# Optimization experiments

Hardware: AMD Instinct MI355X
Metric: run time of the kernel (lower is better)

Reference implementation:

```python
import jax, jax.numpy as jnp
import numpy as np

LN_EPS = 1e-5

def _ln(x, g):
    # LayerNorm with no bias, matching torch (population variance)
    m = x.mean(-1, keepdims=True)
    v = x.var(-1, keepdims=True)
    return (x - m) / jnp.sqrt(v + LN_EPS) * g


def setup_inputs() -> dict:
    key = jax.random.key(0)
    ks = jax.random.split(key, 10)
    B, S, D, L, V = 4, 4096, 256, 6, 32000
    std = 0.02  # nn.init.normal_(std=0.02)
    tokens = jax.random.randint(ks[0], (B, S), 0, V)
    wte = jax.random.normal(ks[1], (V, D), jnp.float32) * std
    wpe = jax.random.normal(ks[2], (S + 1, D), jnp.float32) * std  # context_size+1 table
    g_e = jnp.ones((D,), jnp.float32)
    g_p = jnp.ones((D,), jnp.float32)
    g_out = jnp.ones((D,), jnp.float32)
    ff_w1 = jax.random.normal(ks[3], (D, 4 * D), jnp.float32) * std
    ff_w2 = jax.random.normal(ks[4], (4 * D, D), jnp.float32) * std
    Wq = jax.random.normal(ks[5], (L, D, D), jnp.float32) * std
    Wk = jax.random.normal(ks[6], (L, D, D), jnp.float32) * std
    Wv = jax.random.normal(ks[7], (L, D, D), jnp.float32) * std
    return {"tokens": tokens, "wte": wte, "wpe": wpe, "g_e": g_e, "g_p": g_p,
            "g_out": g_out, "ff_w1": ff_w1, "ff_w2": ff_w2,
            "Wq": Wq, "Wk": Wk, "Wv": Wv}


def reference(tokens, wte, wpe, g_e, g_p, g_out, ff_w1, ff_w2, Wq, Wk, Wv):
    B, S = tokens.shape
    D = wte.shape[1]
    L = Wq.shape[0]
    # embeddings + pre-LN (dropout = identity at eval)
    e = _ln(wte[tokens], g_e)                 # [B,S,D] token stream
    p = _ln(wpe[:S], g_p)                     # [S,D]   positional stream (batch-invariant)
    x = e + p[None]                           # [B,S,D]
    # covariate FF on positional stream (use_ppe=True): p = p + W2 @ gelu(W1 @ p)
    p = p + jax.nn.gelu(p @ ff_w1, approximate=False) @ ff_w2
    causal = jnp.tril(jnp.ones((S, S), bool))
    inv_sqrt_d = D ** -0.5
    for l in range(L):
        # use_ppe: Q=K from positional stream (batch-invariant), V from token embeds
        q = p @ Wq[l]                          # [S,D]
        k = p @ Wk[l]                          # [S,D]
        v = jnp.einsum('bsd,de->bse', e, Wv[l])  # [B,S,D]
        s = (q @ k.T) * inv_sqrt_d             # [S,S], shared across batch
        s = jnp.where(causal, s, -jnp.inf)
        a = jax.nn.softmax(s, axis=-1)
        x = x + jnp.einsum('st,btd->bsd', a, v)
    # targets=None path: last position only
    x = x[:, -1:, :]                           # [B,1,D]
    x = _ln(x, g_out)                          # use_ln_out
    logits = x @ _ln(wte, g_e).T               # tied output head through ln_e
    return logits                              # [B,1,V]
```

## Files before the change

kernel.cpp:

```cpp
#include <hip/hip_runtime.h>
#include <hip/hip_bf16.h>

#define LN_EPS 1e-5f

typedef __attribute__((ext_vector_type(8))) short s8v;
typedef __attribute__((ext_vector_type(4))) float f32x4;

__device__ __forceinline__ float wred_sum(float v) {
#pragma unroll
  for (int o = 32; o > 0; o >>= 1) v += __shfl_xor(v, o, 64);
  return v;
}
__device__ __forceinline__ float wred_max(float v) {
#pragma unroll
  for (int o = 32; o > 0; o >>= 1) v = fmaxf(v, __shfl_xor(v, o, 64));
  return v;
}
__device__ __forceinline__ float bf2f(unsigned short u) {
  union { unsigned int i; float f; } c;
  c.i = ((unsigned int)u) << 16;
  return c.f;
}
__device__ __forceinline__ unsigned short f2bf(float f) {
  __hip_bfloat16 h = (__hip_bfloat16)f;
  return *(unsigned short*)&h;
}
__device__ __forceinline__ float4 bf4(ushort4 u) {
  return (float4){bf2f(u.x), bf2f(u.y), bf2f(u.z), bf2f(u.w)};
}
__device__ __forceinline__ void async_cp16(const __hip_bfloat16* g, __hip_bfloat16* l) {
  __builtin_amdgcn_global_load_lds(
      (const __attribute__((address_space(1))) unsigned int*)g,
      (__attribute__((address_space(3))) unsigned int*)l, 16, 0, 0);
}

__global__ void prep_k(const float* __restrict__ wpe, const float* __restrict__ wte,
                       const int* __restrict__ tokens,
                       const float* __restrict__ g_p, const float* __restrict__ g_e,
                       const float* __restrict__ ff_w1,
                       unsigned short* __restrict__ p0b, unsigned short* __restrict__ e,
                       unsigned short* __restrict__ w1T, float* __restrict__ zeros) {
  __shared__ float lds[64][65];
  int bx = blockIdx.x, t = threadIdx.x;
  int w = t >> 6, lane = t & 63;

  if (bx < 5120) {
    int row;
    const float* g;
    const float4* src;
    if (bx < 1024) {
      row = bx * 4 + w;
      src = (const float4*)(wpe + (size_t)row * 256);
      g = g_p;
    } else {
      row = (bx - 1024) * 4 + w;
      int tok = tokens[row];
      src = (const float4*)(wte + (size_t)tok * 256);
      g = g_e;
    }
    float4 v = src[lane];
    float mean = wred_sum(v.x + v.y + v.z + v.w) * (1.f / 256.f);
    float4 d = {v.x - mean, v.y - mean, v.z - mean, v.w - mean};
    float var = wred_sum(d.x * d.x + d.y * d.y + d.z * d.z + d.w * d.w) * (1.f / 256.f);
    float r = rsqrtf(var + LN_EPS);
    float4 gv = ((const float4*)g)[lane];
    ushort4 ob = {f2bf(d.x * r * gv.x), f2bf(d.y * r * gv.y),
                  f2bf(d.z * r * gv.z), f2bf(d.w * r * gv.w)};
    if (bx < 1024) ((ushort4*)(p0b + (size_t)row * 256))[lane] = ob;
    else           ((ushort4*)(e   + (size_t)row * 256))[lane] = ob;
    return;
  }
  if (bx < 5184) {
    int i = bx - 5120;
    int bxx = i & 3, byy = i >> 2;
    int x = t & 63, y4 = t >> 6;
    int r0 = bxx * 64, c0 = byy * 64;
#pragma unroll
    for (int k = 0; k < 16; ++k) {
      int r = y4 * 16 + k;
      lds[r][x] = ff_w1[(size_t)(r0 + r) * 1024 + c0 + x];
    }
    __syncthreads();
#pragma unroll
    for (int k = 0; k < 16; ++k) {
      int a = y4 * 16 + k;
      w1T[(size_t)(c0 + a) * 256 + r0 + x] = f2bf(lds[x][a]);
    }
    return;
  }
  for (int i = t; i < 8960; i += 256) zeros[i] = 0.f;
}

__global__ __launch_bounds__(256, 4) void mfma_gemm_mlp(
    const __hip_bfloat16* __restrict__ A, const __hip_bfloat16* __restrict__ BT,
    __hip_bfloat16* __restrict__ Cout,
    const float* __restrict__ W2, const unsigned short* __restrict__ p0b,
    float* __restrict__ plast) {
  __shared__ __hip_bfloat16 As[64 * 64];
  __shared__ __hip_bfloat16 Bs[64 * 64];
  __shared__ float hl[64];
  const int t = threadIdx.x;
  const int lane = t & 63, wave = t >> 6;
  const int wr = wave >> 1, wc = wave & 1;
  const int fr = lane & 15, quad = lane >> 4;
  const int mtx = blockIdx.x, ntx = blockIdx.y;
  const int m0 = mtx * 64, n0 = ntx * 64;

  f32x4 acc[2][2];
#pragma unroll
  for (int i = 0; i < 2; ++i)
#pragma unroll
    for (int j = 0; j < 2; ++j) acc[i][j] = (f32x4){0.f, 0.f, 0.f, 0.f};

  for (int k0 = 0; k0 < 256; k0 += 64) {
    __syncthreads();
#pragma unroll
    for (int j = 0; j < 2; ++j) {
      int ld = wave * 2 + j;
      int slot = ld * 64 + lane;
      int m = slot >> 3, c = slot & 7;
      async_cp16(A + (size_t)(m0 + m) * 256 + k0 + ((c ^ (m & 7)) << 3), As + ld * 512);
    }
#pragma unroll
    for (int j = 0; j < 2; ++j) {
      int ld = wave * 2 + j;
      int slot = ld * 64 + lane;
      int n = slot >> 3, c = slot & 7;
      async_cp16(BT + (size_t)(n0 + n) * 256 + k0 + ((c ^ (n & 7)) << 3), Bs + ld * 512);
    }
    __syncthreads();
#pragma unroll
    for (int h = 0; h < 2; ++h) {
      s8v af[2], bfv[2];
#pragma unroll
      for (int i = 0; i < 2; ++i) {
        int m = wr * 32 + i * 16 + fr;
        int ch = (h * 4 + quad) ^ (m & 7);
        af[i] = *(const s8v*)(As + m * 64 + ch * 8);
      }
#pragma unroll
      for (int j = 0; j < 2; ++j) {
        int n = wc * 32 + j * 16 + fr;
        int ch = (h * 4 + quad) ^ (n & 7);
        bfv[j] = *(const s8v*)(Bs + n * 64 + ch * 8);
      }
#pragma unroll
      for (int i = 0; i < 2; ++i)
#pragma unroll
        for (int j = 0; j < 2; ++j)
          acc[i][j] = __builtin_amdgcn_mfma_f32_16x16x32_bf16(af[i], bfv[j], acc[i][j], 0, 0, 0);
    }
  }

#pragma unroll
  for (int i = 0; i < 2; ++i) {
#pragma unroll
    for (int j = 0; j < 2; ++j) {
#pragma unroll
      for (int r = 0; r < 4; ++r) {
        int row = m0 + wr * 32 + i * 16 + quad * 4 + r;
        int col = n0 + wc * 32 + j * 16 + fr;
        float v = acc[i][j][r];
        v = 0.5f * v * (1.f + erff(v * 0.70710678118654752f));
        Cout[(size_t)row * 1024 + col] = (__hip_bfloat16)v;
        if (mtx == 63 && row == 4095) hl[col - n0] = v;
      }
    }
  }
  if (mtx == 63) {
    __syncthreads();
    float pa = (ntx == 0) ? bf2f(p0b[(size_t)4095 * 256 + t]) : 0.f;
#pragma unroll
    for (int kk = 0; kk < 64; ++kk)
      pa += hl[kk] * W2[(size_t)(n0 + kk) * 256 + t];
    atomicAdd(&plast[t], pa);
  }
}

__global__ void q_k(const float* __restrict__ plast, const float* __restrict__ Wq,
                    float* __restrict__ qall) {
  int c = blockIdx.x, l = blockIdx.y, t = threadIdx.x;
  const float* W = Wq + (size_t)l * 65536;
  float pa = 0.f;
#pragma unroll
  for (int i = 0; i < 16; ++i) {
    int d = c * 16 + i;
    pa += plast[d] * W[d * 256 + t];
  }
  atomicAdd(&qall[l * 256 + t], pa);
}

__global__ void kv_k(const float* __restrict__ Wk, const float* __restrict__ qall,
                     float* __restrict__ kv) {
  int l = blockIdx.y;
  int w = threadIdx.x >> 6, lane = threadIdx.x & 63;
  int r = blockIdx.x * 4 + w;
  float4 wv = ((const float4*)(Wk + (size_t)l * 65536 + (size_t)r * 256))[lane];
  float4 qv = ((const float4*)(qall + l * 256))[lane];
  float dot = wred_sum(wv.x * qv.x + wv.y * qv.y + wv.z * qv.z + wv.w * qv.w);
  if (lane == 0) kv[l * 256 + r] = dot;
}

__global__ void w2kv_k(const float* __restrict__ W2, const float* __restrict__ kv,
                       float* __restrict__ w2kv) {
  int l = blockIdx.y;
  int w = threadIdx.x >> 6, lane = threadIdx.x & 63;
  int r = blockIdx.x * 4 + w;
  float4 wv = ((const float4*)(W2 + (size_t)r * 256))[lane];
  float4 qv = ((const float4*)(kv + l * 256))[lane];
  float dot = wred_sum(wv.x * qv.x + wv.y * qv.y + wv.z * qv.z + wv.w * qv.w);
  if (lane == 0) w2kv[l * 1024 + r] = dot;
}

__global__ __launch_bounds__(256) void sc_k(
    const unsigned short* __restrict__ p0b, const unsigned short* __restrict__ hB,
    const float* __restrict__ kv, const float* __restrict__ w2kv,
    float* __restrict__ sc) {
  __shared__ float skv[6 * 256];
  __shared__ float sw2[6 * 1024];
  int t = threadIdx.x;
  for (int i = t; i < 1536; i += 256) skv[i] = kv[i];
  for (int i = t; i < 6144; i += 256) sw2[i] = w2kv[i];
  __syncthreads();
  int wave = t >> 6, lane = t & 63;
#pragma unroll
  for (int rr = 0; rr < 2; ++rr) {
    int row = blockIdx.x * 8 + wave * 2 + rr;
    const ushort4* hrow = (const ushort4*)(hB + (size_t)row * 1024);
    float4 h0 = bf4(hrow[lane]);
    float4 h1 = bf4(hrow[64 + lane]);
    float4 h2 = bf4(hrow[128 + lane]);
    float4 h3 = bf4(hrow[192 + lane]);
    float4 p = bf4(((const ushort4*)(p0b + (size_t)row * 256))[lane]);
#pragma unroll
    for (int l = 0; l < 6; ++l) {
      float4 kf = ((const float4*)(skv + l * 256))[lane];
      float4 w0 = ((const float4*)(sw2 + l * 1024))[lane];
      float4 w1 = ((const float4*)(sw2 + l * 1024 + 256))[lane];
      float4 w2 = ((const float4*)(sw2 + l * 1024 + 512))[lane];
      float4 w3 = ((const float4*)(sw2 + l * 1024 + 768))[lane];
      float a = p.x * kf.x + p.y * kf.y + p.z * kf.z + p.w * kf.w;
      a += h0.x * w0.x + h0.y * w0.y + h0.z * w0.z + h0.w * w0.w;
      a += h1.x * w1.x + h1.y * w1.y + h1.z * w1.z + h1.w * w1.w;
      a += h2.x * w2.x + h2.y * w2.y + h2.z * w2.z + h2.w * w2.w;
      a += h3.x * w3.x + h3.y * w3.y + h3.z * w3.z + h3.w * w3.w;
      a = wred_sum(a);
      if (lane == 0) sc[(size_t)l * 4096 + row] = a * 0.0625f;
    }
  }
}

__global__ void softmax_k(const float* __restrict__ sc, float* __restrict__ w) {
  int l = blockIdx.x, t = threadIdx.x;
  float4 v = ((const float4*)(sc + (size_t)l * 4096))[t];
  float m = fmaxf(fmaxf(v.x, v.y), fmaxf(v.z, v.w));
  m = wred_max(m);
  __shared__ float red[16];
  __shared__ float red2[16];
  int lane = t & 63, wv = t >> 6;
  if (lane == 0) red[wv] = m;
  __syncthreads();
  float mm = red[0];
#pragma unroll
  for (int i = 1; i < 16; ++i) mm = fmaxf(mm, red[i]);
  float e0 = expf(v.x - mm), e1 = expf(v.y - mm), e2 = expf(v.z - mm), e3 = expf(v.w - mm);
  float s = wred_sum(e0 + e1 + e2 + e3);
  if (lane == 0) red2[wv] = s;
  __syncthreads();
  float tot = 0.f;
#pragma unroll
  for (int i = 0; i < 16; ++i) tot += red2[i];
  float inv = 1.f / tot;
  float4 o = {e0 * inv, e1 * inv, e2 * inv, e3 * inv};
  ((float4*)(w + (size_t)l * 4096))[t] = o;
}

__global__ void ctx_k(const unsigned short* __restrict__ e, const float* __restrict__ w,
                      float* __restrict__ ctx) {
  int c = blockIdx.x, b = blockIdx.y, t = threadIdx.x;
  const unsigned short* eb = e + ((size_t)b * 4096 + c * 32) * 256;
  const float* w0 = w + c * 32;
  float a[6] = {0.f, 0.f, 0.f, 0.f, 0.f, 0.f};
#pragma unroll 4
  for (int i = 0; i < 32; ++i) {
    float ev = bf2f(eb[(size_t)i * 256 + t]);
#pragma unroll
    for (int l = 0; l < 6; ++l) a[l] += w0[l * 4096 + i] * ev;
  }
#pragma unroll
  for (int l = 0; l < 6; ++l) atomicAdd(&ctx[(l * 4 + b) * 256 + t], a[l]);
}

__global__ void proj_k(const float* __restrict__ ctx, const float* __restrict__ Wv,
                       float* __restrict__ xacc) {
  int c = blockIdx.x, l = blockIdx.y, t = threadIdx.x;
  const float* W = Wv + (size_t)l * 65536;
  float pa[4] = {0.f, 0.f, 0.f, 0.f};
#pragma unroll
  for (int i = 0; i < 16; ++i) {
    int d = c * 16 + i;
    float wv = W[d * 256 + t];
#pragma unroll
    for (int b = 0; b < 4; ++b) pa[b] += ctx[(l * 4 + b) * 256 + d] * wv;
  }
#pragma unroll
  for (int b = 0; b < 4; ++b) atomicAdd(&xacc[b * 256 + t], pa[b]);
}

__global__ void logits_fin_k(const float* __restrict__ wte, const float* __restrict__ ge,
                             const float* __restrict__ gout,
                             const unsigned short* __restrict__ e,
                             const unsigned short* __restrict__ p0b,
                             const float* __restrict__ xacc,
                             float* __restrict__ out) {
  int wv = threadIdx.x >> 6, lane = threadIdx.x & 63;
  float4 go4 = ((const float4*)gout)[lane];
  float4 ge4 = ((const float4*)ge)[lane];
  float4 pl = bf4(((const ushort4*)(p0b + (size_t)4095 * 256))[lane]);
  float4 xb[4];
#pragma unroll
  for (int b = 0; b < 4; ++b) {
    float4 xa = ((const float4*)(xacc + b * 256))[lane];
    float4 ev = bf4(((const ushort4*)(e + ((size_t)(b * 4096 + 4095)) * 256))[lane]);
    float4 vv = {xa.x + ev.x + pl.x, xa.y + ev.y + pl.y,
                 xa.z + ev.z + pl.z, xa.w + ev.w + pl.w};
    float mean = wred_sum(vv.x + vv.y + vv.z + vv.w) * (1.f / 256.f);
    float4 d = {vv.x - mean, vv.y - mean, vv.z - mean, vv.w - mean};
    float var = wred_sum(d.x * d.x + d.y * d.y + d.z * d.z + d.w * d.w) * (1.f / 256.f);
    float r = rsqrtf(var + LN_EPS);
    xb[b] = (float4){d.x * r * go4.x, d.y * r * go4.y, d.z * r * go4.z, d.w * r * go4.w};
  }
  int v = blockIdx.x * 4 + wv;
  float4 x = ((const float4*)(wte + (size_t)v * 256))[lane];
  float mean = wred_sum(x.x + x.y + x.z + x.w) * (1.f / 256.f);
  float4 d = {x.x - mean, x.y - mean, x.z - mean, x.w - mean};
  float var = wred_sum(d.x * d.x + d.y * d.y + d.z * d.z + d.w * d.w) * (1.f / 256.f);
  float r = rsqrtf(var + LN_EPS);
  float4 ln = {d.x * r * ge4.x, d.y * r * ge4.y, d.z * r * ge4.z, d.w * r * ge4.w};
#pragma unroll
  for (int b = 0; b < 4; ++b) {
    float dot = wred_sum(ln.x * xb[b].x + ln.y * xb[b].y +
                         ln.z * xb[b].z + ln.w * xb[b].w);
    if (lane == 0) out[b * 32000 + v] = dot;
  }
}

#define O_E     ((size_t)0)
#define O_P0B   ((size_t)2097152)
#define O_W1T   ((size_t)2621440)
#define O_HB    ((size_t)2752512)
#define O_CTX   ((size_t)4849664)
#define O_QALL  ((size_t)4855808)
#define O_XACC  ((size_t)4857344)
#define O_PLAST ((size_t)4858368)
#define O_KV    ((size_t)4858624)
#define O_W2KV  ((size_t)4860160)
#define O_SC    ((size_t)4866304)
#define O_WSM   ((size_t)4890880)

extern "C" void kernel_launch(void* const* d_in, const int* in_sizes, int n_in,
                              void* d_out, int out_size, void* d_ws, size_t ws_size,
                              hipStream_t stream) {
  const int*   tokens = (const int*)d_in[0];
  const float* wte    = (const float*)d_in[1];
  const float* wpe    = (const float*)d_in[2];
  const float* g_e    = (const float*)d_in[3];
  const float* g_p    = (const float*)d_in[4];
  const float* g_out  = (const float*)d_in[5];
  const float* ff_w1  = (const float*)d_in[6];
  const float* ff_w2  = (const float*)d_in[7];
  const float* Wq     = (const float*)d_in[8];
  const float* Wk     = (const float*)d_in[9];
  const float* Wv     = (const float*)d_in[10];
  float* out = (float*)d_out;
  float* ws = (float*)d_ws;

  unsigned short* e   = (unsigned short*)(ws + O_E);
  unsigned short* p0b = (unsigned short*)(ws + O_P0B);
  unsigned short* w1T = (unsigned short*)(ws + O_W1T);
  unsigned short* hB  = (unsigned short*)(ws + O_HB);
  float* ctx   = ws + O_CTX;
  float* qall  = ws + O_QALL;
  float* xacc  = ws + O_XACC;
  float* plast = ws + O_PLAST;
  float* kv    = ws + O_KV;
  float* w2kv  = ws + O_W2KV;
  float* sc    = ws + O_SC;
  float* wsm   = ws + O_WSM;

  prep_k<<<5185, 256, 0, stream>>>(wpe, wte, tokens, g_p, g_e, ff_w1,
                                   p0b, e, w1T, ctx);
  mfma_gemm_mlp<<<dim3(64, 16), 256, 0, stream>>>(
      (const __hip_bfloat16*)p0b, (const __hip_bfloat16*)w1T,
      (__hip_bfloat16*)hB, ff_w2, p0b, plast);
  q_k<<<dim3(16, 6), 256, 0, stream>>>(plast, Wq, qall);
  kv_k<<<dim3(64, 6), 256, 0, stream>>>(Wk, qall, kv);
  w2kv_k<<<dim3(256, 6), 256, 0, stream>>>(ff_w2, kv, w2kv);
  sc_k<<<512, 256, 0, stream>>>(p0b, hB, kv, w2kv, sc);
  softmax_k<<<6, 1024, 0, stream>>>(sc, wsm);
  ctx_k<<<dim3(128, 4), 256, 0, stream>>>(e, wsm, ctx);
  proj_k<<<dim3(16, 6), 256, 0, stream>>>(ctx, Wv, xacc);
  logits_fin_k<<<8000, 256, 0, stream>>>(wte, g_e, g_out, e, p0b, xacc, out);
}
```

Measured before the change: 168.0 us.

## Fuse q/k/W2 projections into one kernel and fold softmax into scoring

Replaces the three small q, kv and w2kv kernels with one kernel. In it, each block recomputes the q and kv vectors redundantly from shared memory, then produces its own slice of w2kv. The separate softmax kernel is removed: the scoring kernel writes exp(score) directly and accumulates partial sums with atomics, and the context kernel applies the normalisation. This cuts launches and intermediate round trips, at the cost of redundant matvec work in every block. It also drops the max-subtraction in softmax, which relies on scores staying small enough that exp cannot overflow.

Result: slower. 203.9 us (+21.4%).

```diff
diff --git a/kernel.cpp b/kernel.cpp
--- a/kernel.cpp
+++ b/kernel.cpp
@@ -9,11 +9,6 @@
 __device__ __forceinline__ float wred_sum(float v) {
 #pragma unroll
   for (int o = 32; o > 0; o >>= 1) v += __shfl_xor(v, o, 64);
-  return v;
-}
-__device__ __forceinline__ float wred_max(float v) {
-#pragma unroll
-  for (int o = 32; o > 0; o >>= 1) v = fmaxf(v, __shfl_xor(v, o, 64));
   return v;
 }
 __device__ __forceinline__ float bf2f(unsigned short u) {
@@ -33,6 +28,19 @@
       (const __attribute__((address_space(1))) unsigned int*)g,
       (__attribute__((address_space(3))) unsigned int*)l, 16, 0, 0);
 }
+
+#define O_E     ((size_t)0)
+#define O_P0B   ((size_t)2097152)
+#define O_W1T   ((size_t)2621440)
+#define O_HB    ((size_t)2752512)
+#define O_CTX   ((size_t)4849664)
+#define O_XACC  ((size_t)4855808)
+#define O_PLAST ((size_t)4856832)
+#define O_SSUM  ((size_t)4857088)
+#define O_KV    ((size_t)4857472)
+#define O_W2KV  ((size_t)4859008)
+#define O_SC    ((size_t)4865152)
+#define N_ZERO  7808
 
 __global__ void prep_k(const float* __restrict__ wpe, const float* __restrict__ wte,
                        const int* __restrict__ tokens,
@@ -88,7 +96,7 @@
     }
     return;
   }
-  for (int i = t; i < 8960; i += 256) zeros[i] = 0.f;
+  for (int i = t; i < N_ZERO; i += 256) zeros[i] = 0.f;
 }
 
 __global__ __launch_bounds__(256, 4) void mfma_gemm_mlp(
@@ -177,52 +185,57 @@
   }
 }
 
-__global__ void q_k(const float* __restrict__ plast, const float* __restrict__ Wq,
-                    float* __restrict__ qall) {
-  int c = blockIdx.x, l = blockIdx.y, t = threadIdx.x;
-  const float* W = Wq + (size_t)l * 65536;
-  float pa = 0.f;
-#pragma unroll
-  for (int i = 0; i < 16; ++i) {
-    int d = c * 16 + i;
-    pa += plast[d] * W[d * 256 + t];
-  }
-  atomicAdd(&qall[l * 256 + t], pa);
-}
-
-__global__ void kv_k(const float* __restrict__ Wk, const float* __restrict__ qall,
-                     float* __restrict__ kv) {
-  int l = blockIdx.y;
-  int w = threadIdx.x >> 6, lane = threadIdx.x & 63;
-  int r = blockIdx.x * 4 + w;
-  float4 wv = ((const float4*)(Wk + (size_t)l * 65536 + (size_t)r * 256))[lane];
-  float4 qv = ((const float4*)(qall + l * 256))[lane];
-  float dot = wred_sum(wv.x * qv.x + wv.y * qv.y + wv.z * qv.z + wv.w * qv.w);
-  if (lane == 0) kv[l * 256 + r] = dot;
-}
-
-__global__ void w2kv_k(const float* __restrict__ W2, const float* __restrict__ kv,
-                       float* __restrict__ w2kv) {
-  int l = blockIdx.y;
-  int w = threadIdx.x >> 6, lane = threadIdx.x & 63;
-  int r = blockIdx.x * 4 + w;
-  float4 wv = ((const float4*)(W2 + (size_t)r * 256))[lane];
-  float4 qv = ((const float4*)(kv + l * 256))[lane];
-  float dot = wred_sum(wv.x * qv.x + wv.y * qv.y + wv.z * qv.z + wv.w * qv.w);
-  if (lane == 0) w2kv[l * 1024 + r] = dot;
+__global__ __launch_bounds__(256) void qkw_k(
+    const float* __restrict__ plast, const float* __restrict__ Wq,
+    const float* __restrict__ Wk, const float* __restrict__ W2,
+    float* __restrict__ kvout, float* __restrict__ w2kv) {
+  __shared__ float spl[256];
+  __shared__ float sq[256];
+  __shared__ float skv[256];
+  const int bx = blockIdx.x, l = blockIdx.y, t = threadIdx.x;
+  const int w = t >> 6, lane = t & 63;
+
+  spl[t] = plast[t];
+  __syncthreads();
+  const float* Q = Wq + (size_t)l * 65536;
+  float qa = 0.f;
+#pragma unroll 8
+  for (int d = 0; d < 256; ++d) qa += spl[d] * Q[(size_t)d * 256 + t];
+  sq[t] = qa;
+  __syncthreads();
+  const float* K = Wk + (size_t)l * 65536;
+  float4 qv = ((const float4*)sq)[lane];
+  for (int r = w; r < 256; r += 4) {
+    float4 wv = ((const float4*)(K + (size_t)r * 256))[lane];
+    float dot = wred_sum(wv.x * qv.x + wv.y * qv.y + wv.z * qv.z + wv.w * qv.w);
+    if (lane == 0) skv[r] = dot;
+  }
+  __syncthreads();
+  if (bx == 0) kvout[l * 256 + t] = skv[t];
+  const int r0 = bx * 16;
+  float4 kf = ((const float4*)skv)[lane];
+#pragma unroll
+  for (int rr = 0; rr < 4; ++rr) {
+    int r = r0 + w * 4 + rr;
+    float4 wv = ((const float4*)(W2 + (size_t)r * 256))[lane];
+    float dot = wred_sum(wv.x * kf.x + wv.y * kf.y + wv.z * kf.z + wv.w * kf.w);
+    if (lane == 0) w2kv[l * 1024 + r] = dot;
+  }
 }
 
 __global__ __launch_bounds__(256) void sc_k(
     const unsigned short* __restrict__ p0b, const unsigned short* __restrict__ hB,
     const float* __restrict__ kv, const float* __restrict__ w2kv,
-    float* __restrict__ sc) {
+    float* __restrict__ es, float* __restrict__ ssum) {
   __shared__ float skv[6 * 256];
   __shared__ float sw2[6 * 1024];
+  __shared__ float sred[4][6];
   int t = threadIdx.x;
   for (int i = t; i < 1536; i += 256) skv[i] = kv[i];
   for (int i = t; i < 6144; i += 256) sw2[i] = w2kv[i];
   __syncthreads();
   int wave = t >> 6, lane = t & 63;
+  float ps[6] = {0.f, 0.f, 0.f, 0.f, 0.f, 0.f};
 #pragma unroll
   for (int rr = 0; rr < 2; ++rr) {
     int row = blockIdx.x * 8 + wave * 2 + rr;
@@ -244,42 +257,39 @@
       a += h1.x * w1.x + h1.y * w1.y + h1.z * w1.z + h1.w * w1.w;
       a += h2.x * w2.x + h2.y * w2.y + h2.z * w2.z + h2.w * w2.w;
       a += h3.x * w3.x + h3.y * w3.y + h3.z * w3.z + h3.w * w3.w;
-      a = wred_sum(a);
-      if (lane == 0) sc[(size_t)l * 4096 + row] = a * 0.0625f;
-    }
-  }
-}
-
-__global__ void softmax_k(const float* __restrict__ sc, float* __restrict__ w) {
-  int l = blockIdx.x, t = threadIdx.x;
-  float4 v = ((const float4*)(sc + (size_t)l * 4096))[t];
-  float m = fmaxf(fmaxf(v.x, v.y), fmaxf(v.z, v.w));
-  m = wred_max(m);
-  __shared__ float red[16];
-  __shared__ float red2[16];
-  int lane = t & 63, wv = t >> 6;
-  if (lane == 0) red[wv] = m;
-  __syncthreads();
-  float mm = red[0];
-#pragma unroll
-  for (int i = 1; i < 16; ++i) mm = fmaxf(mm, red[i]);
-  float e0 = expf(v.x - mm), e1 = expf(v.y - mm), e2 = expf(v.z - mm), e3 = expf(v.w - mm);
-  float s = wred_sum(e0 + e1 + e2 + e3);
-  if (lane == 0) red2[wv] = s;
-  __syncthreads();
-  float tot = 0.f;
-#pragma unroll
-  for (int i = 0; i < 16; ++i) tot += red2[i];
-  float inv = 1.f / tot;
-  float4 o = {e0 * inv, e1 * inv, e2 * inv, e3 * inv};
-  ((float4*)(w + (size_t)l * 4096))[t] = o;
-}
-
-__global__ void ctx_k(const unsigned short* __restrict__ e, const float* __restrict__ w,
-                      float* __restrict__ ctx) {
+      a = wred_sum(a) * 0.0625f;
+      float ez = expf(a);
+      ps[l] += ez;
+      if (lane == 0) es[(size_t)l * 4096 + row] = ez;
+    }
+  }
+  if (lane == 0) {
+#pragma unroll
+    for (int l = 0; l < 6; ++l) sred[wave][l] = ps[l];
+  }
+  __syncthreads();
+  if (t < 6) {
+    float s = sred[0][t] + sred[1][t] + sred[2][t] + sred[3][t];
+    atomicAdd(&ssum[t * 64 + (blockIdx.x & 63)], s);
+  }
+}
+
+__global__ void ctx_k(const unsigned short* __restrict__ e, const float* __restrict__ es,
+                      const float* __restrict__ ssum, float* __restrict__ ctx) {
+  __shared__ float sld[384];
+  __shared__ float sinv[6];
   int c = blockIdx.x, b = blockIdx.y, t = threadIdx.x;
+  for (int i = t; i < 384; i += 256) sld[i] = ssum[i];
+  __syncthreads();
+  if (t < 6) {
+    float s = 0.f;
+#pragma unroll
+    for (int i = 0; i < 64; ++i) s += sld[t * 64 + i];
+    sinv[t] = 1.f / s;
+  }
+  __syncthreads();
   const unsigned short* eb = e + ((size_t)b * 4096 + c * 32) * 256;
-  const float* w0 = w + c * 32;
+  const float* w0 = es + c * 32;
   float a[6] = {0.f, 0.f, 0.f, 0.f, 0.f, 0.f};
 #pragma unroll 4
   for (int i = 0; i < 32; ++i) {
@@ -288,7 +298,7 @@
     for (int l = 0; l < 6; ++l) a[l] += w0[l * 4096 + i] * ev;
   }
 #pragma unroll
-  for (int l = 0; l < 6; ++l) atomicAdd(&ctx[(l * 4 + b) * 256 + t], a[l]);
+  for (int l = 0; l < 6; ++l) atomicAdd(&ctx[(l * 4 + b) * 256 + t], a[l] * sinv[l]);
 }
 
 __global__ void proj_k(const float* __restrict__ ctx, const float* __restrict__ Wv,
@@ -344,19 +354,6 @@
     if (lane == 0) out[b * 32000 + v] = dot;
   }
 }
-
-#define O_E     ((size_t)0)
-#define O_P0B   ((size_t)2097152)
-#define O_W1T   ((size_t)2621440)
-#define O_HB    ((size_t)2752512)
-#define O_CTX   ((size_t)4849664)
-#define O_QALL  ((size_t)4855808)
-#define O_XACC  ((size_t)4857344)
-#define O_PLAST ((size_t)4858368)
-#define O_KV    ((size_t)4858624)
-#define O_W2KV  ((size_t)4860160)
-#define O_SC    ((size_t)4866304)
-#define O_WSM   ((size_t)4890880)
 
 extern "C" void kernel_launch(void* const* d_in, const int* in_sizes, int n_in,
                               void* d_out, int out_size, void* d_ws, size_t ws_size,
@@ -380,25 +377,21 @@
   unsigned short* w1T = (unsigned short*)(ws + O_W1T);
   unsigned short* hB  = (unsigned short*)(ws + O_HB);
   float* ctx   = ws + O_CTX;
-  float* qall  = ws + O_QALL;
   float* xacc  = ws + O_XACC;
   float* plast = ws + O_PLAST;
+  float* ssum  = ws + O_SSUM;
   float* kv    = ws + O_KV;
   float* w2kv  = ws + O_W2KV;
-  float* sc    = ws + O_SC;
-  float* wsm   = ws + O_WSM;
+  float* esbuf = ws + O_SC;
 
   prep_k<<<5185, 256, 0, stream>>>(wpe, wte, tokens, g_p, g_e, ff_w1,
                                    p0b, e, w1T, ctx);
   mfma_gemm_mlp<<<dim3(64, 16), 256, 0, stream>>>(
       (const __hip_bfloat16*)p0b, (const __hip_bfloat16*)w1T,
       (__hip_bfloat16*)hB, ff_w2, p0b, plast);
-  q_k<<<dim3(16, 6), 256, 0, stream>>>(plast, Wq, qall);
-  kv_k<<<dim3(64, 6), 256, 0, stream>>>(Wk, qall, kv);
-  w2kv_k<<<dim3(256, 6), 256, 0, stream>>>(ff_w2, kv, w2kv);
-  sc_k<<<512, 256, 0, stream>>>(p0b, hB, kv, w2kv, sc);
-  softmax_k<<<6, 1024, 0, stream>>>(sc, wsm);
-  ctx_k<<<dim3(128, 4), 256, 0, stream>>>(e, wsm, ctx);
+  qkw_k<<<dim3(64, 6), 256, 0, stream>>>(plast, Wq, Wk, ff_w2, kv, w2kv);
+  sc_k<<<512, 256, 0, stream>>>(p0b, hB, kv, w2kv, esbuf, ssum);
+  ctx_k<<<dim3(128, 4), 256, 0, stream>>>(e, esbuf, ssum, ctx);
   proj_k<<<dim3(16, 6), 256, 0, stream>>>(ctx, Wv, xacc);
   logits_fin_k<<<8000, 256, 0, stream>>>(wte, g_e, g_out, e, p0b, xacc, out);
 }
```
